# Kernel tuning notes

Hardware: AMD Instinct MI355X
Metric: run time of the kernel (lower is better)

Reference implementation:

```python
import jax, jax.numpy as jnp
import numpy as np

N_NODES = 50000
IN_DIM = 128
HIDDEN = 64
OUT_DIM = 3
HEADS1 = 4
NEG_SLOPE = 0.2
EPS = 1e-16


def _glorot(key, shape):
    fan_in, fan_out = shape[0], shape[-1]
    lim = (6.0 / (fan_in + fan_out)) ** 0.5
    return jax.random.uniform(key, shape, jnp.float32, -lim, lim)


def setup_inputs() -> dict:
    key = jax.random.key(0)
    ks = jax.random.split(key, 12)
    x = jax.random.normal(ks[0], (N_NODES, IN_DIM), jnp.float32)
    edge_index = jax.random.randint(ks[1], (2, 400000), 0, N_NODES, jnp.int64)
    # layer 1: GATConv(in=128, out=64, heads=4)
    W1 = _glorot(ks[2], (IN_DIM, HEADS1 * HIDDEN))
    att_src1 = _glorot(ks[3], (HEADS1, HIDDEN))
    att_dst1 = _glorot(ks[4], (HEADS1, HIDDEN))
    b1 = jnp.zeros((HEADS1 * HIDDEN,), jnp.float32)
    # layer 2: GATConv(in=256, out=64, heads=1)
    W2 = _glorot(ks[5], (HEADS1 * HIDDEN, HIDDEN))
    att_src2 = _glorot(ks[6], (1, HIDDEN))
    att_dst2 = _glorot(ks[7], (1, HIDDEN))
    b2 = jnp.zeros((HIDDEN,), jnp.float32)
    # output linear
    Wout = _glorot(ks[8], (HIDDEN, OUT_DIM))
    bout = jnp.zeros((OUT_DIM,), jnp.float32)
    return {"x": x, "edge_index": edge_index, "W1": W1, "att_src1": att_src1,
            "att_dst1": att_dst1, "b1": b1, "W2": W2, "att_src2": att_src2,
            "att_dst2": att_dst2, "b2": b2, "Wout": Wout, "bout": bout}


def gat_conv(x, src, dst, W, a_src, a_dst, b, n_nodes):
    H, C = a_src.shape
    h = (x @ W).reshape(n_nodes, H, C)            # [N,H,C]
    a_s = jnp.sum(h * a_src[None], axis=-1)        # [N,H]
    a_d = jnp.sum(h * a_dst[None], axis=-1)        # [N,H]
    e = jax.nn.leaky_relu(a_s[src] + a_d[dst], NEG_SLOPE)  # [E,H]
    # segment softmax over incoming edges of each dst node
    m = jax.ops.segment_max(e, dst, num_segments=n_nodes)
    ex = jnp.exp(e - m[dst])
    denom = jax.ops.segment_sum(ex, dst, num_segments=n_nodes)
    alpha = ex / (denom[dst] + EPS)                # [E,H]
    msg = h[src] * alpha[..., None]                # [E,H,C]
    out = jax.ops.segment_sum(msg, dst, num_segments=n_nodes)
    return out.reshape(n_nodes, H * C) + b


def reference(x, edge_index, W1, att_src1, att_dst1, b1, W2, att_src2, att_dst2, b2, Wout, bout):
    n = x.shape[0]
    loop = jnp.arange(n, dtype=edge_index.dtype)
    src = jnp.concatenate([edge_index[0], loop])   # add self loops (PyG default)
    dst = jnp.concatenate([edge_index[1], loop])
    h = gat_conv(x, src, dst, W1, att_src1, att_dst1, b1, n)
    h = jax.nn.elu(h)
    h = gat_conv(h, src, dst, W2, att_src2, att_dst2, b2, n)
    h = jax.nn.elu(h)
    return h @ Wout + bout
```

## Files before the change

### kernel.cpp

```cpp
#include <hip/hip_runtime.h>
#include <hip/hip_bf16.h>
#include <math.h>

#define N_NODES  50000
#define IN_DIM   128
#define HIDDEN   64
#define OUT_DIM  3
#define HEADS1   4
#define E_RAW    400000
#define E_TOT    450000
#define NEG_SLOPE 0.2f
#define SCAN_CHUNK 1024
#define N_CHUNKS ((N_NODES + SCAN_CHUNK - 1) / SCAN_CHUNK)

typedef __attribute__((ext_vector_type(8))) short bf16x8;
typedef __attribute__((ext_vector_type(4))) float f32x4;

static __device__ __forceinline__ float bfu(unsigned short u) {
    return __uint_as_float(((unsigned)u) << 16);
}
static __device__ __forceinline__ unsigned short f2b_bits(float v) {
    __hip_bfloat16 b = __float2bfloat16(v);
    return *reinterpret_cast<unsigned short*>(&b);
}

static __device__ __forceinline__ void get_edge(const int* __restrict__ ei, int is64,
                                                int e, int& s, int& d) {
    if (e >= E_RAW) { s = d = e - E_RAW; return; }
    if (is64) { s = ei[2 * e]; d = ei[2 * E_RAW + 2 * e]; }
    else      { s = ei[e];     d = ei[E_RAW + e]; }
    s = min(max(s, 0), N_NODES - 1);
    d = min(max(d, 0), N_NODES - 1);
}

__global__ void detect_int64_kernel(const int* __restrict__ ei, int* __restrict__ flag) {
    __shared__ int any_nonzero;
    if (threadIdx.x == 0) any_nonzero = 0;
    __syncthreads();
    for (int i = threadIdx.x; i < 8192; i += blockDim.x) {
        int k = i * 48;
        if (ei[2 * k + 1] != 0) any_nonzero = 1;
    }
    __syncthreads();
    if (threadIdx.x == 0) flag[0] = (any_nonzero == 0) ? 1 : 0;
}

__global__ void count_deg_kernel(const int* __restrict__ ei, const int* __restrict__ flag,
                                 int* __restrict__ deg) {
    int e = blockIdx.x * blockDim.x + threadIdx.x;
    if (e >= E_TOT) return;
    int s, d;
    get_edge(ei, flag[0], e, s, d);
    atomicAdd(&deg[d], 1);
}

__global__ void scan_local_kernel(const int* __restrict__ deg, int* __restrict__ row_ptr,
                                  int* __restrict__ bsums) {
    __shared__ int buf[SCAN_CHUNK];
    int base = blockIdx.x * SCAN_CHUNK;
    int i = base + threadIdx.x;
    buf[threadIdx.x] = (i < N_NODES) ? deg[i] : 0;
    __syncthreads();
    for (int off = 1; off < SCAN_CHUNK; off <<= 1) {
        int t = (threadIdx.x >= off) ? buf[threadIdx.x - off] : 0;
        __syncthreads();
        buf[threadIdx.x] += t;
        __syncthreads();
    }
    if (i < N_NODES) row_ptr[i + 1] = buf[threadIdx.x];
    if (threadIdx.x == SCAN_CHUNK - 1) bsums[blockIdx.x] = buf[SCAN_CHUNK - 1];
    if (blockIdx.x == 0 && threadIdx.x == 0) row_ptr[0] = 0;
}

__global__ void scan_bsums_kernel(int* __restrict__ bsums) {
    __shared__ int buf[64];
    int i = threadIdx.x;
    buf[i] = (i < N_CHUNKS) ? bsums[i] : 0;
    __syncthreads();
    for (int off = 1; off < 64; off <<= 1) {
        int t = (i >= off) ? buf[i - off] : 0;
        __syncthreads();
        buf[i] += t;
        __syncthreads();
    }
    if (i < N_CHUNKS) bsums[i] = (i == 0) ? 0 : buf[i - 1];
}

__global__ void scan_add_kernel(int* __restrict__ row_ptr, const int* __restrict__ bsums,
                                const int* __restrict__ deg, int* __restrict__ cursor) {
    int i = blockIdx.x * blockDim.x + threadIdx.x;
    if (i < N_NODES) {
        int incl = row_ptr[i + 1] + bsums[i / SCAN_CHUNK];
        row_ptr[i + 1] = incl;
        cursor[i] = incl - deg[i];
    }
}

__global__ void scatter_kernel(const int* __restrict__ ei, const int* __restrict__ flag,
                               int* __restrict__ cursor, int* __restrict__ csr_src) {
    int e = blockIdx.x * blockDim.x + threadIdx.x;
    if (e >= E_TOT) return;
    int s, d;
    get_edge(ei, flag[0], e, s, d);
    int pos = atomicAdd(&cursor[d], 1);
    csr_src[pos] = s;
}

__global__ void wprep_kernel(const float* __restrict__ W1, __hip_bfloat16* __restrict__ W1T,
                             const float* __restrict__ W2, __hip_bfloat16* __restrict__ W2T) {
    int i = blockIdx.x * blockDim.x + threadIdx.x;
    if (i < 256 * 128) {
        int n = i >> 7, k = i & 127;
        *((unsigned short*)W1T + i) = f2b_bits(W1[k * 256 + n]);
    }
    if (i < 64 * 256) {
        int n = i >> 8, k = i & 255;
        *((unsigned short*)W2T + i) = f2b_bits(W2[k * 64 + n]);
    }
}

__global__ void __launch_bounds__(256) gemm_l1_mfma_kernel(
        const float* __restrict__ x, const __hip_bfloat16* __restrict__ W1T,
        const float* __restrict__ att_s, const float* __restrict__ att_d,
        __hip_bfloat16* __restrict__ h1,
        float* __restrict__ asb4, float* __restrict__ adb4) {
    __shared__ unsigned short As[16][136];
    const int tid = threadIdx.x;
    const int wave = tid >> 6, lane = tid & 63;
    const int quad = lane >> 4, m = lane & 15;
    const int row0 = blockIdx.x * 16;
    {
        int r = tid >> 4, seg = tid & 15;
        const float* xa = x + (size_t)(row0 + r) * IN_DIM + seg * 8;
        float4 u = *(const float4*)xa;
        float4 v = *(const float4*)(xa + 4);
        ushort4 p0, p1;
        p0.x = f2b_bits(u.x); p0.y = f2b_bits(u.y); p0.z = f2b_bits(u.z); p0.w = f2b_bits(u.w);
        p1.x = f2b_bits(v.x); p1.y = f2b_bits(v.y); p1.z = f2b_bits(v.z); p1.w = f2b_bits(v.w);
        *(ushort4*)&As[r][seg * 8]     = p0;
        *(ushort4*)&As[r][seg * 8 + 4] = p1;
    }
    __syncthreads();
    const int n0w = wave * 64;
    f32x4 acc0 = {0.f, 0.f, 0.f, 0.f}, acc1 = acc0, acc2 = acc0, acc3 = acc0;
    #pragma unroll
    for (int k0 = 0; k0 < IN_DIM; k0 += 32) {
        int kk = k0 + quad * 8;
        bf16x8 a = *(const bf16x8*)&As[m][kk];
        bf16x8 b0 = *(const bf16x8*)(W1T + (size_t)(n0w +  0 + m) * IN_DIM + kk);
        bf16x8 b1 = *(const bf16x8*)(W1T + (size_t)(n0w + 16 + m) * IN_DIM + kk);
        bf16x8 b2 = *(const bf16x8*)(W1T + (size_t)(n0w + 32 + m) * IN_DIM + kk);
        bf16x8 b3 = *(const bf16x8*)(W1T + (size_t)(n0w + 48 + m) * IN_DIM + kk);
        acc0 = __builtin_amdgcn_mfma_f32_16x16x32_bf16(a, b0, acc0, 0, 0, 0);
        acc1 = __builtin_amdgcn_mfma_f32_16x16x32_bf16(a, b1, acc1, 0, 0, 0);
        acc2 = __builtin_amdgcn_mfma_f32_16x16x32_bf16(a, b2, acc2, 0, 0, 0);
        acc3 = __builtin_amdgcn_mfma_f32_16x16x32_bf16(a, b3, acc3, 0, 0, 0);
    }
    float ats0 = att_s[n0w +  0 + m], atd0 = att_d[n0w +  0 + m];
    float ats1 = att_s[n0w + 16 + m], atd1 = att_d[n0w + 16 + m];
    float ats2 = att_s[n0w + 32 + m], atd2 = att_d[n0w + 32 + m];
    float ats3 = att_s[n0w + 48 + m], atd3 = att_d[n0w + 48 + m];
    unsigned short* out = (unsigned short*)h1;
    #pragma unroll
    for (int i = 0; i < 4; i++) {
        int grow = row0 + quad * 4 + i;
        size_t base = (size_t)grow * 256;
        out[base + n0w +  0 + m] = f2b_bits(acc0[i]);
        out[base + n0w + 16 + m] = f2b_bits(acc1[i]);
        out[base + n0w + 32 + m] = f2b_bits(acc2[i]);
        out[base + n0w + 48 + m] = f2b_bits(acc3[i]);
        float ps = acc0[i] * ats0 + acc1[i] * ats1 + acc2[i] * ats2 + acc3[i] * ats3;
        float pd = acc0[i] * atd0 + acc1[i] * atd1 + acc2[i] * atd2 + acc3[i] * atd3;
        #pragma unroll
        for (int off = 1; off < 16; off <<= 1) {
            ps += __shfl_xor(ps, off, 16);
            pd += __shfl_xor(pd, off, 16);
        }
        if (m == 0) {
            asb4[grow * 4 + wave] = ps;
            adb4[grow * 4 + wave] = pd;
        }
    }
}

__global__ void attn_score1_kernel(const __hip_bfloat16* __restrict__ h2,
                                   const float* __restrict__ att_s,
                                   const float* __restrict__ att_d,
                                   float* __restrict__ asb, float* __restrict__ adb) {
    int n = blockIdx.x * blockDim.x + threadIdx.x;
    if (n >= N_NODES) return;
    const unsigned short* row = (const unsigned short*)h2 + (size_t)n * 64;
    float s = 0.f, d = 0.f;
    #pragma unroll
    for (int c4 = 0; c4 < 16; c4++) {
        ushort4 f = *(const ushort4*)(row + c4 * 4);
        float4 as_ = *(const float4*)(att_s + c4 * 4);
        float4 ad_ = *(const float4*)(att_d + c4 * 4);
        s += bfu(f.x) * as_.x + bfu(f.y) * as_.y + bfu(f.z) * as_.z + bfu(f.w) * as_.w;
        d += bfu(f.x) * ad_.x + bfu(f.y) * ad_.y + bfu(f.z) * ad_.z + bfu(f.w) * ad_.w;
    }
    asb[n] = s;
    adb[n] = d;
}

__global__ void __launch_bounds__(256) gemm_l2_mfma_kernel(
        const __hip_bfloat16* __restrict__ eluagg, const __hip_bfloat16* __restrict__ W2T,
        __hip_bfloat16* __restrict__ h2) {
    const int tid = threadIdx.x;
    const int wave = tid >> 6, lane = tid & 63;
    const int quad = lane >> 4, m = lane & 15;
    const int row0 = blockIdx.x * 16;
    const int n0 = wave * 16;
    f32x4 acc = {0.f, 0.f, 0.f, 0.f};
    #pragma unroll
    for (int k0 = 0; k0 < 256; k0 += 32) {
        int kk = k0 + quad * 8;
        bf16x8 a = *(const bf16x8*)(eluagg + (size_t)(row0 + m) * 256 + kk);
        bf16x8 b = *(const bf16x8*)(W2T + (size_t)(n0 + m) * 256 + kk);
        acc = __builtin_amdgcn_mfma_f32_16x16x32_bf16(a, b, acc, 0, 0, 0);
    }
    unsigned short* out = (unsigned short*)h2;
    #pragma unroll
    for (int i = 0; i < 4; i++) {
        int grow = row0 + quad * 4 + i;
        out[(size_t)grow * 64 + n0 + m] = f2b_bits(acc[i]);
    }
}

__global__ void softmax_stats4_kernel(const int* __restrict__ row_ptr,
                                      const int* __restrict__ csr_src,
                                      const float* __restrict__ asb4,
                                      const float* __restrict__ adb4,
                                      float* __restrict__ wT,
                                      float* __restrict__ inv_l) {
    int n = blockIdx.x * blockDim.x + threadIdx.x;
    if (n >= N_NODES) return;
    int b = row_ptr[n], e = row_ptr[n + 1];
    float4 adn = ((const float4*)adb4)[n];
    float4 l = make_float4(0.f, 0.f, 0.f, 0.f);
    for (int j = b; j < e; j++) {
        int s = csr_src[j];
        float4 v = ((const float4*)asb4)[s];
        v.x += adn.x; v.y += adn.y; v.z += adn.z; v.w += adn.w;
        v.x = (v.x > 0.f) ? v.x : NEG_SLOPE * v.x;
        v.y = (v.y > 0.f) ? v.y : NEG_SLOPE * v.y;
        v.z = (v.z > 0.f) ? v.z : NEG_SLOPE * v.z;
        v.w = (v.w > 0.f) ? v.w : NEG_SLOPE * v.w;
        float4 p;
        p.x = __expf(v.x); p.y = __expf(v.y); p.z = __expf(v.z); p.w = __expf(v.w);
        wT[0 * E_TOT + j] = p.x;
        wT[1 * E_TOT + j] = p.y;
        wT[2 * E_TOT + j] = p.z;
        wT[3 * E_TOT + j] = p.w;
        l.x += p.x; l.y += p.y; l.z += p.z; l.w += p.w;
    }
    float4 il;
    il.x = 1.f / (l.x + 1e-16f); il.y = 1.f / (l.y + 1e-16f);
    il.z = 1.f / (l.z + 1e-16f); il.w = 1.f / (l.w + 1e-16f);
    ((float4*)inv_l)[n] = il;
}

__global__ void softmax_stats1_kernel(const int* __restrict__ row_ptr,
                                      const int* __restrict__ csr_src,
                                      const float* __restrict__ as_,
                                      const float* __restrict__ ad_,
                                      float* __restrict__ wT,
                                      float* __restrict__ inv_l) {
    int n = blockIdx.x * blockDim.x + threadIdx.x;
    if (n >= N_NODES) return;
    int b = row_ptr[n], e = row_ptr[n + 1];
    float adn = ad_[n];
    float l = 0.f;
    for (int j = b; j < e; j++) {
        float v = as_[csr_src[j]] + adn;
        v = (v > 0.f) ? v : NEG_SLOPE * v;
        float p = __expf(v);
        wT[j] = p;
        l += p;
    }
    inv_l[n] = 1.f / (l + 1e-16f);
}

__global__ void __launch_bounds__(256) gat_gather4_kernel(
        const int* __restrict__ row_ptr, const int* __restrict__ csr_src,
        const float* __restrict__ wT, const float* __restrict__ inv_l,
        const __hip_bfloat16* __restrict__ h1, const float* __restrict__ bias,
        __hip_bfloat16* __restrict__ eluagg) {
    int wave = threadIdx.x >> 6;
    int lane = threadIdx.x & 63;
    int n = blockIdx.x * 4 + wave;
    if (n >= N_NODES) return;
    int b = row_ptr[n], e = row_ptr[n + 1];
    int head = lane >> 4;
    const float* wTh = wT + (size_t)head * E_TOT;
    float4 a0 = make_float4(0, 0, 0, 0), a1 = a0, a2 = a0, a3 = a0;
    int j = b;
    for (; j + 4 <= e; j += 4) {
        int s0 = csr_src[j], s1 = csr_src[j + 1], s2 = csr_src[j + 2], s3 = csr_src[j + 3];
        float w0 = wTh[j], w1 = wTh[j + 1], w2 = wTh[j + 2], w3 = wTh[j + 3];
        ushort4 f0 = *(const ushort4*)(h1 + (size_t)s0 * 256 + lane * 4);
        ushort4 f1 = *(const ushort4*)(h1 + (size_t)s1 * 256 + lane * 4);
        ushort4 f2 = *(const ushort4*)(h1 + (size_t)s2 * 256 + lane * 4);
        ushort4 f3 = *(const ushort4*)(h1 + (size_t)s3 * 256 + lane * 4);
        a0.x += w0 * bfu(f0.x); a0.y += w0 * bfu(f0.y); a0.z += w0 * bfu(f0.z); a0.w += w0 * bfu(f0.w);
        a1.x += w1 * bfu(f1.x); a1.y += w1 * bfu(f1.y); a1.z += w1 * bfu(f1.z); a1.w += w1 * bfu(f1.w);
        a2.x += w2 * bfu(f2.x); a2.y += w2 * bfu(f2.y); a2.z += w2 * bfu(f2.z); a2.w += w2 * bfu(f2.w);
        a3.x += w3 * bfu(f3.x); a3.y += w3 * bfu(f3.y); a3.z += w3 * bfu(f3.z); a3.w += w3 * bfu(f3.w);
    }
    for (; j < e; j++) {
        int s = csr_src[j];
        float w = wTh[j];
        ushort4 f = *(const ushort4*)(h1 + (size_t)s * 256 + lane * 4);
        a0.x += w * bfu(f.x); a0.y += w * bfu(f.y); a0.z += w * bfu(f.z); a0.w += w * bfu(f.w);
    }
    float il = inv_l[n * 4 + head];
    float4 bb = *(const float4*)(bias + lane * 4);
    float4 r;
    r.x = (a0.x + a1.x + a2.x + a3.x) * il + bb.x;
    r.y = (a0.y + a1.y + a2.y + a3.y) * il + bb.y;
    r.z = (a0.z + a1.z + a2.z + a3.z) * il + bb.z;
    r.w = (a0.w + a1.w + a2.w + a3.w) * il + bb.w;
    r.x = (r.x > 0.f) ? r.x : expm1f(r.x);
    r.y = (r.y > 0.f) ? r.y : expm1f(r.y);
    r.z = (r.z > 0.f) ? r.z : expm1f(r.z);
    r.w = (r.w > 0.f) ? r.w : expm1f(r.w);
    ushort4 st;
    st.x = f2b_bits(r.x); st.y = f2b_bits(r.y); st.z = f2b_bits(r.z); st.w = f2b_bits(r.w);
    *(ushort4*)(eluagg + (size_t)n * 256 + lane * 4) = st;
}

__global__ void __launch_bounds__(256) gat_gather1_out_kernel(
        const int* __restrict__ row_ptr, const int* __restrict__ csr_src,
        const float* __restrict__ wT, const float* __restrict__ inv_l,
        const __hip_bfloat16* __restrict__ h2, const float* __restrict__ bias,
        const float* __restrict__ Wout, const float* __restrict__ bout,
        float* __restrict__ out) {
    int wave = threadIdx.x >> 6;
    int lane = threadIdx.x & 63;
    int n = blockIdx.x * 4 + wave;
    if (n >= N_NODES) return;
    int b = row_ptr[n], e = row_ptr[n + 1];
    int cg = lane & 15, slot = lane >> 4;
    float4 acc = make_float4(0, 0, 0, 0);
    for (int j0 = b; j0 < e; j0 += 4) {
        int j = j0 + slot;
        float w = 0.f; int s = 0;
        if (j < e) { s = csr_src[j]; w = wT[j]; }
        ushort4 f = *(const ushort4*)(h2 + (size_t)s * 64 + cg * 4);
        acc.x += w * bfu(f.x); acc.y += w * bfu(f.y);
        acc.z += w * bfu(f.z); acc.w += w * bfu(f.w);
    }
    acc.x += __shfl_xor(acc.x, 16, 64); acc.y += __shfl_xor(acc.y, 16, 64);
    acc.z += __shfl_xor(acc.z, 16, 64); acc.w += __shfl_xor(acc.w, 16, 64);
    acc.x += __shfl_xor(acc.x, 32, 64); acc.y += __shfl_xor(acc.y, 32, 64);
    acc.z += __shfl_xor(acc.z, 32, 64); acc.w += __shfl_xor(acc.w, 32, 64);
    float il = inv_l[n];
    float4 bb = *(const float4*)(bias + cg * 4);
    float4 v;
    v.x = acc.x * il + bb.x; v.y = acc.y * il + bb.y;
    v.z = acc.z * il + bb.z; v.w = acc.w * il + bb.w;
    v.x = (v.x > 0.f) ? v.x : expm1f(v.x);
    v.y = (v.y > 0.f) ? v.y : expm1f(v.y);
    v.z = (v.z > 0.f) ? v.z : expm1f(v.z);
    v.w = (v.w > 0.f) ? v.w : expm1f(v.w);
    int c0 = cg * 4;
    float o0 = v.x * Wout[(c0+0)*OUT_DIM+0] + v.y * Wout[(c0+1)*OUT_DIM+0]
             + v.z * Wout[(c0+2)*OUT_DIM+0] + v.w * Wout[(c0+3)*OUT_DIM+0];
    float o1 = v.x * Wout[(c0+0)*OUT_DIM+1] + v.y * Wout[(c0+1)*OUT_DIM+1]
             + v.z * Wout[(c0+2)*OUT_DIM+1] + v.w * Wout[(c0+3)*OUT_DIM+1];
    float o2 = v.x * Wout[(c0+0)*OUT_DIM+2] + v.y * Wout[(c0+1)*OUT_DIM+2]
             + v.z * Wout[(c0+2)*OUT_DIM+2] + v.w * Wout[(c0+3)*OUT_DIM+2];
    #pragma unroll
    for (int off = 1; off < 16; off <<= 1) {
        o0 += __shfl_xor(o0, off, 64);
        o1 += __shfl_xor(o1, off, 64);
        o2 += __shfl_xor(o2, off, 64);
    }
    if (lane == 0) {
        out[n * OUT_DIM + 0] = o0 + bout[0];
        out[n * OUT_DIM + 1] = o1 + bout[1];
        out[n * OUT_DIM + 2] = o2 + bout[2];
    }
}

extern "C" void kernel_launch(void* const* d_in, const int* in_sizes, int n_in,
                              void* d_out, int out_size, void* d_ws, size_t ws_size,
                              hipStream_t stream) {
    const float* x    = (const float*)d_in[0];
    const int*   ei   = (const int*)d_in[1];
    const float* W1   = (const float*)d_in[2];
    const float* as1  = (const float*)d_in[3];
    const float* ad1  = (const float*)d_in[4];
    const float* b1   = (const float*)d_in[5];
    const float* W2   = (const float*)d_in[6];
    const float* as2  = (const float*)d_in[7];
    const float* ad2  = (const float*)d_in[8];
    const float* b2v  = (const float*)d_in[9];
    const float* Wout = (const float*)d_in[10];
    const float* bout = (const float*)d_in[11];
    float* out = (float*)d_out;

    float* ws    = (float*)d_ws;
    int*   flag  = (int*)ws;
    float* asb4  = ws + 16;
    float* adb4  = asb4 + (size_t)N_NODES * 4;
    float* ilb4  = adb4 + (size_t)N_NODES * 4;
    float* asb1  = ilb4 + (size_t)N_NODES * 4;
    float* adb1  = asb1 + N_NODES;
    float* ilb1  = adb1 + N_NODES;
    float* wT    = ilb1 + N_NODES;
    __hip_bfloat16* h1     = (__hip_bfloat16*)(wT + (size_t)E_TOT * 4);
    __hip_bfloat16* eluagg = (__hip_bfloat16*)(h1 + (size_t)N_NODES * 256);
    __hip_bfloat16* h2     = (__hip_bfloat16*)(eluagg + (size_t)N_NODES * 256);
    __hip_bfloat16* W1T    = (__hip_bfloat16*)(h2 + (size_t)N_NODES * 64);
    __hip_bfloat16* W2T    = W1T + 256 * 128;
    int* deg     = (int*)(W2T + 64 * 256);
    int* bsums   = deg + N_NODES;
    int* row_ptr = bsums + 64;
    int* cursor  = row_ptr + N_NODES + 16;
    int* csr_src = cursor + N_NODES;

    const int EB = (E_TOT + 255) / 256;
    const int NB = (N_NODES + 255) / 256;
    const int AB = (N_NODES + 3) / 4;
    const int MB = N_NODES / 16;

    detect_int64_kernel<<<1, 256, 0, stream>>>(ei, flag);

    hipMemsetAsync(deg, 0, (size_t)N_NODES * sizeof(int), stream);
    count_deg_kernel<<<EB, 256, 0, stream>>>(ei, flag, deg);
    scan_local_kernel<<<N_CHUNKS, SCAN_CHUNK, 0, stream>>>(deg, row_ptr, bsums);
    scan_bsums_kernel<<<1, 64, 0, stream>>>(bsums);
    scan_add_kernel<<<NB, 256, 0, stream>>>(row_ptr, bsums, deg, cursor);
    scatter_kernel<<<EB, 256, 0, stream>>>(ei, flag, cursor, csr_src);

    wprep_kernel<<<(256 * 128 + 255) / 256, 256, 0, stream>>>(W1, W1T, W2, W2T);
    gemm_l1_mfma_kernel<<<MB, 256, 0, stream>>>(x, W1T, as1, ad1, h1, asb4, adb4);
    softmax_stats4_kernel<<<NB, 256, 0, stream>>>(row_ptr, csr_src, asb4, adb4, wT, ilb4);
    gat_gather4_kernel<<<AB, 256, 0, stream>>>(row_ptr, csr_src, wT, ilb4, h1, b1, eluagg);

    gemm_l2_mfma_kernel<<<MB, 256, 0, stream>>>(eluagg, W2T, h2);
    attn_score1_kernel<<<NB, 256, 0, stream>>>(h2, as2, ad2, asb1, adb1);
    softmax_stats1_kernel<<<NB, 256, 0, stream>>>(row_ptr, csr_src, asb1, adb1, wT, ilb1);

    gat_gather1_out_kernel<<<AB, 256, 0, stream>>>(row_ptr, csr_src, wT, ilb1, h2,
                                                   b2v, Wout, bout, out);
}
```

Before: 301.9 us.

## Fuse weight prep into degree count, fold layer-2 attention scores into GEMM, unroll gather

Merges the weight transpose/bf16 conversion into the degree-counting launch and computes layer-2 attention scores inside the layer-2 MFMA GEMM epilogue using shuffles and a shared-memory reduction, removing two kernel launches and a re-read of h2. The layer-1 gather loop is unrolled from 4 to 8 edges per iteration to keep more independent loads in flight. The trade-offs are higher register pressure in the gather and an extra block barrier in the GEMM. Attention scores are now computed from fp32 accumulators instead of bf16-rounded h2, a small numerical change.

```diff
diff --git a/kernel.cpp b/kernel.cpp
--- a/kernel.cpp
+++ b/kernel.cpp
@@ -12,6 +12,7 @@
 #define NEG_SLOPE 0.2f
 #define SCAN_CHUNK 1024
 #define N_CHUNKS ((N_NODES + SCAN_CHUNK - 1) / SCAN_CHUNK)
+#define WPREP_BLOCKS 128
 
 typedef __attribute__((ext_vector_type(8))) short bf16x8;
 typedef __attribute__((ext_vector_type(4))) float f32x4;
@@ -45,9 +46,24 @@
     if (threadIdx.x == 0) flag[0] = (any_nonzero == 0) ? 1 : 0;
 }
 
-__global__ void count_deg_kernel(const int* __restrict__ ei, const int* __restrict__ flag,
-                                 int* __restrict__ deg) {
-    int e = blockIdx.x * blockDim.x + threadIdx.x;
+__global__ void wprep_count_kernel(const float* __restrict__ W1, __hip_bfloat16* __restrict__ W1T,
+                                   const float* __restrict__ W2, __hip_bfloat16* __restrict__ W2T,
+                                   const int* __restrict__ ei, const int* __restrict__ flag,
+                                   int* __restrict__ deg) {
+    int bid = blockIdx.x;
+    if (bid < WPREP_BLOCKS) {
+        int i = bid * 256 + threadIdx.x;
+        if (i < 256 * 128) {
+            int n = i >> 7, k = i & 127;
+            *((unsigned short*)W1T + i) = f2b_bits(W1[k * 256 + n]);
+        }
+        if (i < 64 * 256) {
+            int n = i >> 8, k = i & 255;
+            *((unsigned short*)W2T + i) = f2b_bits(W2[k * 64 + n]);
+        }
+        return;
+    }
+    int e = (bid - WPREP_BLOCKS) * 256 + threadIdx.x;
     if (e >= E_TOT) return;
     int s, d;
     get_edge(ei, flag[0], e, s, d);
@@ -104,19 +120,6 @@
     get_edge(ei, flag[0], e, s, d);
     int pos = atomicAdd(&cursor[d], 1);
     csr_src[pos] = s;
-}
-
-__global__ void wprep_kernel(const float* __restrict__ W1, __hip_bfloat16* __restrict__ W1T,
-                             const float* __restrict__ W2, __hip_bfloat16* __restrict__ W2T) {
-    int i = blockIdx.x * blockDim.x + threadIdx.x;
-    if (i < 256 * 128) {
-        int n = i >> 7, k = i & 127;
-        *((unsigned short*)W1T + i) = f2b_bits(W1[k * 256 + n]);
-    }
-    if (i < 64 * 256) {
-        int n = i >> 8, k = i & 255;
-        *((unsigned short*)W2T + i) = f2b_bits(W2[k * 64 + n]);
-    }
 }
 
 __global__ void __launch_bounds__(256) gemm_l1_mfma_kernel(
@@ -183,29 +186,13 @@
     }
 }
 
-__global__ void attn_score1_kernel(const __hip_bfloat16* __restrict__ h2,
-                                   const float* __restrict__ att_s,
-                                   const float* __restrict__ att_d,
-                                   float* __restrict__ asb, float* __restrict__ adb) {
-    int n = blockIdx.x * blockDim.x + threadIdx.x;
-    if (n >= N_NODES) return;
-    const unsigned short* row = (const unsigned short*)h2 + (size_t)n * 64;
-    float s = 0.f, d = 0.f;
-    #pragma unroll
-    for (int c4 = 0; c4 < 16; c4++) {
-        ushort4 f = *(const ushort4*)(row + c4 * 4);
-        float4 as_ = *(const float4*)(att_s + c4 * 4);
-        float4 ad_ = *(const float4*)(att_d + c4 * 4);
-        s += bfu(f.x) * as_.x + bfu(f.y) * as_.y + bfu(f.z) * as_.z + bfu(f.w) * as_.w;
-        d += bfu(f.x) * ad_.x + bfu(f.y) * ad_.y + bfu(f.z) * ad_.z + bfu(f.w) * ad_.w;
-    }
-    asb[n] = s;
-    adb[n] = d;
-}
-
 __global__ void __launch_bounds__(256) gemm_l2_mfma_kernel(
         const __hip_bfloat16* __restrict__ eluagg, const __hip_bfloat16* __restrict__ W2T,
-        __hip_bfloat16* __restrict__ h2) {
+        const float* __restrict__ att_s, const float* __restrict__ att_d,
+        __hip_bfloat16* __restrict__ h2,
+        float* __restrict__ asb, float* __restrict__ adb) {
+    __shared__ float sPS[4][16];
+    __shared__ float sPD[4][16];
     const int tid = threadIdx.x;
     const int wave = tid >> 6, lane = tid & 63;
     const int quad = lane >> 4, m = lane & 15;
@@ -219,11 +206,30 @@
         bf16x8 b = *(const bf16x8*)(W2T + (size_t)(n0 + m) * 256 + kk);
         acc = __builtin_amdgcn_mfma_f32_16x16x32_bf16(a, b, acc, 0, 0, 0);
     }
+    float ats = att_s[n0 + m], atd = att_d[n0 + m];
     unsigned short* out = (unsigned short*)h2;
     #pragma unroll
     for (int i = 0; i < 4; i++) {
         int grow = row0 + quad * 4 + i;
         out[(size_t)grow * 64 + n0 + m] = f2b_bits(acc[i]);
+        float ps = acc[i] * ats;
+        float pd = acc[i] * atd;
+        #pragma unroll
+        for (int off = 1; off < 16; off <<= 1) {
+            ps += __shfl_xor(ps, off, 16);
+            pd += __shfl_xor(pd, off, 16);
+        }
+        if (m == 0) {
+            sPS[wave][quad * 4 + i] = ps;
+            sPD[wave][quad * 4 + i] = pd;
+        }
+    }
+    __syncthreads();
+    if (tid < 16) {
+        float ps = sPS[0][tid] + sPS[1][tid] + sPS[2][tid] + sPS[3][tid];
+        float pd = sPD[0][tid] + sPD[1][tid] + sPD[2][tid] + sPD[3][tid];
+        asb[row0 + tid] = ps;
+        adb[row0 + tid] = pd;
     }
 }
 
@@ -295,17 +301,27 @@
     const float* wTh = wT + (size_t)head * E_TOT;
     float4 a0 = make_float4(0, 0, 0, 0), a1 = a0, a2 = a0, a3 = a0;
     int j = b;
-    for (; j + 4 <= e; j += 4) {
-        int s0 = csr_src[j], s1 = csr_src[j + 1], s2 = csr_src[j + 2], s3 = csr_src[j + 3];
-        float w0 = wTh[j], w1 = wTh[j + 1], w2 = wTh[j + 2], w3 = wTh[j + 3];
+    for (; j + 8 <= e; j += 8) {
+        int s0 = csr_src[j],     s1 = csr_src[j + 1], s2 = csr_src[j + 2], s3 = csr_src[j + 3];
+        int s4 = csr_src[j + 4], s5 = csr_src[j + 5], s6 = csr_src[j + 6], s7 = csr_src[j + 7];
+        float w0 = wTh[j],     w1 = wTh[j + 1], w2 = wTh[j + 2], w3 = wTh[j + 3];
+        float w4 = wTh[j + 4], w5 = wTh[j + 5], w6 = wTh[j + 6], w7 = wTh[j + 7];
         ushort4 f0 = *(const ushort4*)(h1 + (size_t)s0 * 256 + lane * 4);
         ushort4 f1 = *(const ushort4*)(h1 + (size_t)s1 * 256 + lane * 4);
         ushort4 f2 = *(const ushort4*)(h1 + (size_t)s2 * 256 + lane * 4);
         ushort4 f3 = *(const ushort4*)(h1 + (size_t)s3 * 256 + lane * 4);
+        ushort4 f4 = *(const ushort4*)(h1 + (size_t)s4 * 256 + lane * 4);
+        ushort4 f5 = *(const ushort4*)(h1 + (size_t)s5 * 256 + lane * 4);
+        ushort4 f6 = *(const ushort4*)(h1 + (size_t)s6 * 256 + lane * 4);
+        ushort4 f7 = *(const ushort4*)(h1 + (size_t)s7 * 256 + lane * 4);
         a0.x += w0 * bfu(f0.x); a0.y += w0 * bfu(f0.y); a0.z += w0 * bfu(f0.z); a0.w += w0 * bfu(f0.w);
         a1.x += w1 * bfu(f1.x); a1.y += w1 * bfu(f1.y); a1.z += w1 * bfu(f1.z); a1.w += w1 * bfu(f1.w);
         a2.x += w2 * bfu(f2.x); a2.y += w2 * bfu(f2.y); a2.z += w2 * bfu(f2.z); a2.w += w2 * bfu(f2.w);
         a3.x += w3 * bfu(f3.x); a3.y += w3 * bfu(f3.y); a3.z += w3 * bfu(f3.z); a3.w += w3 * bfu(f3.w);
+        a0.x += w4 * bfu(f4.x); a0.y += w4 * bfu(f4.y); a0.z += w4 * bfu(f4.z); a0.w += w4 * bfu(f4.w);
+        a1.x += w5 * bfu(f5.x); a1.y += w5 * bfu(f5.y); a1.z += w5 * bfu(f5.z); a1.w += w5 * bfu(f5.w);
+        a2.x += w6 * bfu(f6.x); a2.y += w6 * bfu(f6.y); a2.z += w6 * bfu(f6.z); a2.w += w6 * bfu(f6.w);
+        a3.x += w7 * bfu(f7.x); a3.y += w7 * bfu(f7.y); a3.z += w7 * bfu(f7.z); a3.w += w7 * bfu(f7.w);
     }
     for (; j < e; j++) {
         int s = csr_src[j];
@@ -426,21 +442,19 @@
     const int MB = N_NODES / 16;
 
     detect_int64_kernel<<<1, 256, 0, stream>>>(ei, flag);
-
     hipMemsetAsync(deg, 0, (size_t)N_NODES * sizeof(int), stream);
-    count_deg_kernel<<<EB, 256, 0, stream>>>(ei, flag, deg);
+
+    wprep_count_kernel<<<WPREP_BLOCKS + EB, 256, 0, stream>>>(W1, W1T, W2, W2T, ei, flag, deg);
     scan_local_kernel<<<N_CHUNKS, SCAN_CHUNK, 0, stream>>>(deg, row_ptr, bsums);
     scan_bsums_kernel<<<1, 64, 0, stream>>>(bsums);
     scan_add_kernel<<<NB, 256, 0, stream>>>(row_ptr, bsums, deg, cursor);
     scatter_kernel<<<EB, 256, 0, stream>>>(ei, flag, cursor, csr_src);
 
-    wprep_kernel<<<(256 * 128 + 255) / 256, 256, 0, stream>>>(W1, W1T, W2, W2T);
     gemm_l1_mfma_kernel<<<MB, 256, 0, stream>>>(x, W1T, as1, ad1, h1, asb4, adb4);
     softmax_stats4_kernel<<<NB, 256, 0, stream>>>(row_ptr, csr_src, asb4, adb4, wT, ilb4);
     gat_gather4_kernel<<<AB, 256, 0, stream>>>(row_ptr, csr_src, wT, ilb4, h1, b1, eluagg);
 
-    gemm_l2_mfma_kernel<<<MB, 256, 0, stream>>>(eluagg, W2T, h2);
-    attn_score1_kernel<<<NB, 256, 0, stream>>>(h2, as2, ad2, asb1, adb1);
+    gemm_l2_mfma_kernel<<<MB, 256, 0, stream>>>(eluagg, W2T, as2, ad2, h2, asb1, adb1);
     softmax_stats1_kernel<<<NB, 256, 0, stream>>>(row_ptr, csr_src, asb1, adb1, wT, ilb1);
 
     gat_gather1_out_kernel<<<AB, 256, 0, stream>>>(row_ptr, csr_src, wT, ilb1, h2,
```

New measurement: 307.9 us. About the same (+2.0%).
